# Kernel tuning notes

Measured on AMD Instinct MI355X. Metric: run time of the kernel, lower is better.

Reference implementation:

```python
import jax, jax.numpy as jnp
import numpy as np

WIDTH = 2048
NUM_HEADS = 16
HEAD_DIM = WIDTH // NUM_HEADS  # 128
ROPE_DIMS = HEAD_DIM // 2      # 64, partial rotary
WINDOW = 512
ROPE_BASE = 10000.0
NEG_INF = -1e9


def apply_rope(x, dims, offset=0, base=ROPE_BASE):
    # x: [B, H, L, hd]; non-traditional (half-split) rotary on first `dims` dims.
    L = x.shape[2]
    half = dims // 2
    pos = (offset + jnp.arange(L)).astype(x.dtype)                     # [L]
    inv_freq = jnp.exp(-jnp.log(jnp.asarray(base, x.dtype)) * (jnp.arange(0, dims, 2).astype(x.dtype) / dims))  # [half]
    theta = pos[:, None] * inv_freq[None, :]                           # [L, half]
    cos = jnp.cos(theta)[None, None]                                   # [1,1,L,half]
    sin = jnp.sin(theta)[None, None]
    x1 = x[..., :half]
    x2 = x[..., half:dims]
    rest = x[..., dims:]
    rx1 = x1 * cos - x2 * sin
    rx2 = x1 * sin + x2 * cos
    return jnp.concatenate([rx1, rx2, rest], axis=-1)


def setup_inputs() -> dict:
    key = jax.random.key(0)
    ks = jax.random.split(key, 6)
    B, L, D, hd = 2, 2048, WIDTH, HEAD_DIM
    x = jax.random.normal(ks[0], (B, L, D), dtype=jnp.float32)
    Wq = jax.random.normal(ks[1], (D, D), dtype=jnp.float32) * 0.02
    Wk = jax.random.normal(ks[2], (D, hd), dtype=jnp.float32) * 0.02
    Wv = jax.random.normal(ks[3], (D, hd), dtype=jnp.float32) * 0.02
    Wo = jax.random.normal(ks[4], (D, D), dtype=jnp.float32) * 0.02
    bo = jax.random.normal(ks[5], (D,), dtype=jnp.float32) * 0.02
    return {"x": x, "Wq": Wq, "Wk": Wk, "Wv": Wv, "Wo": Wo, "bo": bo}


def reference(x, Wq, Wk, Wv, Wo, bo):
    B, L, D = x.shape
    H, hd = NUM_HEADS, HEAD_DIM
    scale = hd ** (-0.5)

    q = (x @ Wq).reshape(B, L, H, hd).transpose(0, 2, 1, 3)   # [B,H,L,hd]
    k = (x @ Wk).reshape(B, L, 1, hd).transpose(0, 2, 1, 3)   # [B,1,L,hd] (MQA)
    v = (x @ Wv).reshape(B, L, 1, hd).transpose(0, 2, 1, 3)

    q = apply_rope(q, ROPE_DIMS)
    k = apply_rope(k, ROPE_DIMS)

    # sliding-window causal mask: attend iff 0 <= i - j < WINDOW
    i = jnp.arange(L)[:, None]
    j = jnp.arange(L)[None, :]
    allowed = (i - j >= 0) & (i - j < WINDOW)                  # [L,L]
    mask = jnp.where(allowed, 0.0, NEG_INF).astype(x.dtype)

    scores = jnp.einsum("bhqd,bkd->bhqk", q, k[:, 0]) * scale  # [B,H,L,L]
    scores = scores + mask[None, None]
    attn = jax.nn.softmax(scores, axis=-1)
    out = jnp.einsum("bhqk,bkd->bhqd", attn, v[:, 0])          # [B,H,L,hd]
    out = out.transpose(0, 2, 1, 3).reshape(B, L, D)
    return out @ Wo + bo
```

## Files before the change

kernel.cpp:

```cpp
#include <hip/hip_runtime.h>
#include <hip/hip_bf16.h>
#include <stdint.h>


typedef float  f32x4  __attribute__((ext_vector_type(4)));
typedef __bf16 bf16x8 __attribute__((ext_vector_type(8)));

#define ASYNC_LD16(gp, lp)                                                     \
  __builtin_amdgcn_global_load_lds(                                            \
      (__attribute__((address_space(1))) void*)(gp),                           \
      (__attribute__((address_space(3))) void*)(lp), 16, 0, 0)

__global__ __launch_bounds__(256) void prep_all(
    const float* __restrict__ x, __hip_bfloat16* __restrict__ xb,
    const float* __restrict__ Wq, const float* __restrict__ Wk,
    const float* __restrict__ Wv, const float* __restrict__ Wo,
    __hip_bfloat16* __restrict__ wqkvT, __hip_bfloat16* __restrict__ woT) {
  __shared__ float t[32][33];
  int bid = blockIdx.x;
  if (bid < 8192) {
    const int i = bid * 256 + threadIdx.x;
    const float4 v = ((const float4*)x)[i];
    __align__(8) __hip_bfloat16 o[4] = {
        __float2bfloat16(v.x), __float2bfloat16(v.y),
        __float2bfloat16(v.z), __float2bfloat16(v.w)};
    *(uint2*)(xb + (size_t)i * 4) = *(uint2*)o;
    return;
  }
  bid -= 8192;
  const float* src;
  __hip_bfloat16* dst;
  int C, cb, rb;
  if (bid < 4096) {
    src = Wq; dst = wqkvT; C = 2048; cb = bid & 63; rb = bid >> 6;
  } else if (bid < 4352) {
    const int l = bid - 4096;
    src = Wk; dst = wqkvT + 2048ull * 2048; C = 128; cb = l & 3; rb = l >> 2;
  } else if (bid < 4608) {
    const int l = bid - 4352;
    src = Wv; dst = wqkvT + 2176ull * 2048; C = 128; cb = l & 3; rb = l >> 2;
  } else {
    const int l = bid - 4608;
    src = Wo; dst = woT; C = 2048; cb = l & 63; rb = l >> 6;
  }
  const int c0 = cb * 32, r0 = rb * 32;
  const int xx = threadIdx.x & 31, y = threadIdx.x >> 5;
#pragma unroll
  for (int i = 0; i < 32; i += 8)
    t[y + i][xx] = src[(size_t)(r0 + y + i) * C + c0 + xx];
  __syncthreads();
#pragma unroll
  for (int i = 0; i < 32; i += 8)
    dst[(size_t)(c0 + y + i) * 2048 + r0 + xx] = __float2bfloat16(t[xx][y + i]);
}

__device__ __forceinline__ void xcd_remap(int& bx, int& by) {
  const int nwg = gridDim.x * gridDim.y;
  const int flat = blockIdx.y * gridDim.x + blockIdx.x;
  const int cpx = nwg >> 3;
  const int nid = (flat & 7) * cpx + (flat >> 3);
  bx = nid % gridDim.x;
  by = nid / gridDim.x;
}

__device__ __forceinline__ void gemm_core64(const __bf16* __restrict__ A,
                                            const __bf16* __restrict__ BT,
                                            int K, int m0, int n0, __bf16* As,
                                            __bf16* Bs, f32x4 (&acc)[2][4]) {
  const int tid = threadIdx.x;
  const int wave = tid >> 6;
  const int lane = tid & 63;
  const int wm = (wave & 3) * 32;
  const int wn = (wave >> 2) * 64;
  const int ln = lane & 15;
  const int quad = lane >> 4;
  const int rdoff = (quad ^ ((ln >> 1) & 3)) * 8;

  size_t goff[2];
  int ldsoff[2];
#pragma unroll
  for (int i = 0; i < 2; i++) {
    const int cidx = (wave * 2 + i) * 64 + lane;
    const int p = cidx >> 9;
    const int pidx = cidx & 511;
    const int row = pidx >> 2;
    const int cc = pidx & 3;
    const int cg = cc ^ ((row >> 1) & 3);
    goff[i] = (size_t)row * K + p * 32 + cg * 8;
    ldsoff[i] = (wave * 2 + i) * 512;
  }
  const __bf16* Abase = A + (size_t)m0 * K;
  const __bf16* Bbase = BT + (size_t)n0 * K;

  for (int k0 = 0; k0 < K; k0 += 64) {
#pragma unroll
    for (int i = 0; i < 2; i++)
      ASYNC_LD16(Abase + k0 + goff[i], As + ldsoff[i]);
#pragma unroll
    for (int i = 0; i < 2; i++)
      ASYNC_LD16(Bbase + k0 + goff[i], Bs + ldsoff[i]);
    __syncthreads();
    bf16x8 af[2][2], bf[4][2];
#pragma unroll
    for (int i = 0; i < 2; i++)
#pragma unroll
      for (int p = 0; p < 2; p++)
        af[i][p] = *(const bf16x8*)&As[p * 4096 + (wm + i * 16 + ln) * 32 + rdoff];
#pragma unroll
    for (int j = 0; j < 4; j++)
#pragma unroll
      for (int p = 0; p < 2; p++)
        bf[j][p] = *(const bf16x8*)&Bs[p * 4096 + (wn + j * 16 + ln) * 32 + rdoff];
#pragma unroll
    for (int p = 0; p < 2; p++)
#pragma unroll
      for (int i = 0; i < 2; i++)
#pragma unroll
        for (int j = 0; j < 4; j++)
          acc[i][j] = __builtin_amdgcn_mfma_f32_16x16x32_bf16(af[i][p], bf[j][p],
                                                              acc[i][j], 0, 0, 0);
    __syncthreads();
  }
}

__global__ __launch_bounds__(512) void gemm_qkv(
    const __bf16* __restrict__ A, const __bf16* __restrict__ BT,
    __hip_bfloat16* __restrict__ qd, __hip_bfloat16* __restrict__ kd,
    __hip_bfloat16* __restrict__ vtd, int K) {
  __shared__ __align__(16) __bf16 As[128 * 64];
  __shared__ __align__(16) __bf16 Bs[128 * 64];
  int bx, by;
  xcd_remap(bx, by);
  const int m0 = by * 128;
  const int n0 = bx * 128;
  f32x4 acc[2][4];
  const f32x4 zero = {0.f, 0.f, 0.f, 0.f};
#pragma unroll
  for (int i = 0; i < 2; i++)
#pragma unroll
    for (int j = 0; j < 4; j++) acc[i][j] = zero;
  gemm_core64(A, BT, K, m0, n0, As, Bs, acc);

  const int tid = threadIdx.x;
  const int wave = tid >> 6;
  const int lane = tid & 63;
  const int quad = lane >> 4;
  const int ln = lane & 15;
  const int wm = (wave & 3) * 32;
  const int wn = (wave >> 2) * 64;

  if (n0 == 2176) {
    const int bb = m0 >> 11;
    const int mloc = m0 & 2047;
#pragma unroll
    for (int i = 0; i < 2; i++) {
      const int rb = mloc + wm + i * 16 + quad * 4;
#pragma unroll
      for (int j = 0; j < 4; j++) {
        const int col = wn + j * 16 + ln;
        __align__(8) __hip_bfloat16 t4[4];
#pragma unroll
        for (int r = 0; r < 4; r++) t4[r] = __float2bfloat16(acc[i][j][r]);
        *(uint2*)(vtd + ((size_t)(bb * 128 + col)) * 2048 + rb) = *(uint2*)t4;
      }
    }
    return;
  }

  __hip_bfloat16* dst;
  int dstride, dcol;
  if (n0 < 2048) {
    dst = qd; dstride = 2048; dcol = n0;
  } else {
    dst = kd; dstride = 128; dcol = 0;
  }
  const bool dorope = (wn == 0);
  float invf0 = 0.f, invf1 = 0.f;
  if (dorope) {
    invf0 = expf(-0.28782313662425574f * (float)ln);
    invf1 = expf(-0.28782313662425574f * (float)(16 + ln));
  }

#pragma unroll
  for (int i = 0; i < 2; i++) {
#pragma unroll
    for (int r = 0; r < 4; r++) {
      const int row = m0 + wm + i * 16 + quad * 4 + r;
      float o0 = acc[i][0][r], o1 = acc[i][1][r];
      float o2 = acc[i][2][r], o3 = acc[i][3][r];
      if (dorope) {
        const float pos = (float)(row & 2047);
        float s0, c0, s1, c1;
        __sincosf(pos * invf0, &s0, &c0);
        __sincosf(pos * invf1, &s1, &c1);
        const float a0 = o0, b0 = o2, a1 = o1, b1 = o3;
        o0 = a0 * c0 - b0 * s0;
        o2 = a0 * s0 + b0 * c0;
        o1 = a1 * c1 - b1 * s1;
        o3 = a1 * s1 + b1 * c1;
      }
      __hip_bfloat16* rp = dst + (size_t)row * dstride + dcol + wn + ln;
      rp[0]  = __float2bfloat16(o0);
      rp[16] = __float2bfloat16(o1);
      rp[32] = __float2bfloat16(o2);
      rp[48] = __float2bfloat16(o3);
    }
  }
}

__global__ __launch_bounds__(512) void gemm_out(
    const __bf16* __restrict__ A, const __bf16* __restrict__ BT,
    float* __restrict__ C, const float* __restrict__ bias, int N, int K) {
  __shared__ __align__(16) __bf16 As[128 * 64];
  __shared__ __align__(16) __bf16 Bs[128 * 64];
  int bx, by;
  xcd_remap(bx, by);
  const int m0 = by * 128;
  const int n0 = bx * 128;
  f32x4 acc[2][4];
  const f32x4 zero = {0.f, 0.f, 0.f, 0.f};
#pragma unroll
  for (int i = 0; i < 2; i++)
#pragma unroll
    for (int j = 0; j < 4; j++) acc[i][j] = zero;
  gemm_core64(A, BT, K, m0, n0, As, Bs, acc);

  const int tid = threadIdx.x;
  const int wave = tid >> 6;
  const int lane = tid & 63;
  const int wm = (wave & 3) * 32;
  const int wn = (wave >> 2) * 64;
  const int lrow = lane & 15;
#pragma unroll
  for (int j = 0; j < 4; j++) {
    const int col = n0 + wn + j * 16 + lrow;
    const float bv = bias[col];
#pragma unroll
    for (int i = 0; i < 2; i++) {
#pragma unroll
      for (int r = 0; r < 4; r++) {
        const int row = m0 + wm + i * 16 + (lane >> 4) * 4 + r;
        C[(size_t)row * N + col] = acc[i][j][r] + bv;
      }
    }
  }
}

__global__ __launch_bounds__(256) void attn_mfma(
    const __bf16* __restrict__ qb,
    const __bf16* __restrict__ kb,
    const __bf16* __restrict__ vtb,
    __hip_bfloat16* __restrict__ o)
{
  __shared__ __align__(16) __bf16 Ks[4][64 * 32];
  __shared__ __align__(16) __bf16 Vs[2][128 * 32];
  __shared__ __align__(16) __bf16 Ps[4][2][2][512];
  const int tid = threadIdx.x;
  const int wave = tid >> 6;
  const int lane = tid & 63;
  const int quad = lane >> 4;
  const int ln = lane & 15;
  const int bid = blockIdx.x;
  const int q0 = (bid & 15) * 128;
  const int h = (bid >> 4) & 15;
  const int b = bid >> 8;
  const int swr = (ln >> 1) & 3;
  const int rdoff = (quad ^ swr) * 8;

  bf16x8 qf[2][4];
#pragma unroll
  for (int g = 0; g < 2; g++) {
    const __bf16* qrow =
        qb + ((size_t)(b * 2048 + q0 + wave * 32 + g * 16 + ln)) * 2048 + h * 128;
#pragma unroll
    for (int ks = 0; ks < 4; ks++)
      qf[g][ks] = *(const bf16x8*)(qrow + ks * 32 + quad * 8);
  }

  f32x4 oacc[2][8];
  const f32x4 zero = {0.f, 0.f, 0.f, 0.f};
#pragma unroll
  for (int g = 0; g < 2; g++)
#pragma unroll
    for (int nb = 0; nb < 8; nb++) oacc[g][nb] = zero;
  float li[2][4] = {{0.f, 0.f, 0.f, 0.f}, {0.f, 0.f, 0.f, 0.f}};
  const float scale = 0.08838834764831845f;

  const __bf16* kbase = kb + (size_t)b * 2048 * 128;
  const __bf16* vbase = vtb + (size_t)b * 128 * 2048;

  const int tstart = (q0 >= 512) ? 0 : (512 - q0) / 64;
  for (int t = tstart; t < 10; ++t) {
    const int jt = q0 - 512 + 64 * t;
    __syncthreads();
    {
      const int key4 = lane >> 2, uu = lane & 3;
      const int sw = (key4 >> 1) & 3;
#pragma unroll
      for (int i = 0; i < 4; ++i) {
        const int c = wave * 4 + i;
        const int ks = c & 3, keybase = (c >> 2) * 16;
        ASYNC_LD16(kbase + (size_t)(jt + keybase + key4) * 128 + ks * 32 +
                       (uu ^ sw) * 8,
                   &Ks[ks][keybase * 32]);
      }
#pragma unroll
      for (int i = 0; i < 4; ++i) {
        const int c = wave * 4 + i;
        const int p = c & 1, dbase = (c >> 1) * 16;
        ASYNC_LD16(vbase + (size_t)(dbase + key4) * 2048 + jt + p * 32 +
                       (uu ^ sw) * 8,
                   &Vs[p][dbase * 32]);
      }
    }
    __syncthreads();

    f32x4 sacc[2][4];
#pragma unroll
    for (int g = 0; g < 2; g++)
#pragma unroll
      for (int j = 0; j < 4; j++) sacc[g][j] = zero;
#pragma unroll
    for (int j = 0; j < 4; j++)
#pragma unroll
      for (int ks = 0; ks < 4; ks++) {
        const bf16x8 kf = *(const bf16x8*)&Ks[ks][(j * 16 + ln) * 32 + rdoff];
#pragma unroll
        for (int g = 0; g < 2; g++)
          sacc[g][j] = __builtin_amdgcn_mfma_f32_16x16x32_bf16(qf[g][ks], kf,
                                                               sacc[g][j], 0, 0, 0);
      }

#pragma unroll
    for (int g = 0; g < 2; g++)
#pragma unroll
      for (int j = 0; j < 4; j++)
#pragma unroll
        for (int r = 0; r < 4; r++) {
          float v = sacc[g][j][r] * scale;
          const int d0 = (wave * 32 + g * 16 + quad * 4 + r) - (j * 16 + ln);
          if (t <= 1 && d0 >= (t << 6)) v = -1e30f;
          if (t >= 8 && d0 < ((t - 8) << 6)) v = -1e30f;
          v = fminf(v, 60.f);
          const float p = __expf(v);
          li[g][r] += p;
          const int ch = (j & 1) * 2 + (ln >> 3);
          const int swp = (quad * 2 + (r >> 1)) & 3;
          Ps[wave][g][j >> 1]
            [(quad * 4 + r) * 32 + (ch ^ swp) * 8 + (ln & 7)] = (__bf16)p;
        }

    const bf16x8 pf00 = *(const bf16x8*)&Ps[wave][0][0][ln * 32 + rdoff];
    const bf16x8 pf01 = *(const bf16x8*)&Ps[wave][0][1][ln * 32 + rdoff];
    const bf16x8 pf10 = *(const bf16x8*)&Ps[wave][1][0][ln * 32 + rdoff];
    const bf16x8 pf11 = *(const bf16x8*)&Ps[wave][1][1][ln * 32 + rdoff];
#pragma unroll
    for (int nb = 0; nb < 8; nb++) {
      const bf16x8 vf0 = *(const bf16x8*)&Vs[0][(nb * 16 + ln) * 32 + rdoff];
      const bf16x8 vf1 = *(const bf16x8*)&Vs[1][(nb * 16 + ln) * 32 + rdoff];
      oacc[0][nb] =
          __builtin_amdgcn_mfma_f32_16x16x32_bf16(pf00, vf0, oacc[0][nb], 0, 0, 0);
      oacc[0][nb] =
          __builtin_amdgcn_mfma_f32_16x16x32_bf16(pf01, vf1, oacc[0][nb], 0, 0, 0);
      oacc[1][nb] =
          __builtin_amdgcn_mfma_f32_16x16x32_bf16(pf10, vf0, oacc[1][nb], 0, 0, 0);
      oacc[1][nb] =
          __builtin_amdgcn_mfma_f32_16x16x32_bf16(pf11, vf1, oacc[1][nb], 0, 0, 0);
    }
  }

#pragma unroll
  for (int off = 1; off < 16; off <<= 1)
#pragma unroll
    for (int g = 0; g < 2; g++)
#pragma unroll
      for (int r = 0; r < 4; r++) li[g][r] += __shfl_xor(li[g][r], off);

#pragma unroll
  for (int g = 0; g < 2; g++) {
    __hip_bfloat16* obase =
        o + ((size_t)(b * 2048 + q0 + wave * 32 + g * 16 + quad * 4)) * 2048 +
        h * 128 + ln;
#pragma unroll
    for (int r = 0; r < 4; r++) {
      const float inv = 1.0f / li[g][r];
#pragma unroll
      for (int nb = 0; nb < 8; nb++)
        obase[(size_t)r * 2048 + nb * 16] = __float2bfloat16(oacc[g][nb][r] * inv);
    }
  }
}

extern "C" void kernel_launch(void* const* d_in, const int* in_sizes, int n_in,
                              void* d_out, int out_size, void* d_ws,
                              size_t ws_size, hipStream_t stream) {
  const float* x = (const float*)d_in[0];
  const float* Wq = (const float*)d_in[1];
  const float* Wk = (const float*)d_in[2];
  const float* Wv = (const float*)d_in[3];
  const float* Wo = (const float*)d_in[4];
  const float* bo = (const float*)d_in[5];
  float* out = (float*)d_out;

  char* w = (char*)d_ws;
  auto alloc = [&](size_t bytes) {
    void* p = (void*)w;
    w += (bytes + 255) & ~(size_t)255;
    return p;
  };
  __bf16* xb = (__bf16*)alloc(4096ull * 2048 * 2);
  __hip_bfloat16* wqkvT = (__hip_bfloat16*)alloc(2304ull * 2048 * 2);
  __hip_bfloat16* woT = (__hip_bfloat16*)alloc(2048ull * 2048 * 2);
  __hip_bfloat16* qbuf = (__hip_bfloat16*)alloc(4096ull * 2048 * 2);
  __hip_bfloat16* kbuf = (__hip_bfloat16*)alloc(4096ull * 128 * 2);
  __hip_bfloat16* vtb = (__hip_bfloat16*)alloc(4096ull * 128 * 2);
  __hip_bfloat16* attnb = (__hip_bfloat16*)xb;

  prep_all<<<16896, 256, 0, stream>>>(x, (__hip_bfloat16*)xb, Wq, Wk, Wv, Wo,
                                      wqkvT, woT);

  gemm_qkv<<<dim3(18, 32), 512, 0, stream>>>(xb, (const __bf16*)wqkvT, qbuf,
                                             kbuf, vtb, 2048);

  attn_mfma<<<512, 256, 0, stream>>>((const __bf16*)qbuf, (const __bf16*)kbuf,
                                     (const __bf16*)vtb, attnb);

  gemm_out<<<dim3(16, 32), 512, 0, stream>>>((const __bf16*)attnb,
                                             (const __bf16*)woT, out, bo, 2048,
                                             2048);
}
```

Measured before the change: 264.3 us.

## Double-buffer LDS tiles in GEMMs and attention and specialize mask-free softmax

```diff
diff --git a/kernel.cpp b/kernel.cpp
--- a/kernel.cpp
+++ b/kernel.cpp
@@ -63,10 +63,10 @@
   by = nid / gridDim.x;
 }
 
-__device__ __forceinline__ void gemm_core64(const __bf16* __restrict__ A,
-                                            const __bf16* __restrict__ BT,
-                                            int K, int m0, int n0, __bf16* As,
-                                            __bf16* Bs, f32x4 (&acc)[2][4]) {
+__device__ __forceinline__ void gemm_core_db(const __bf16* __restrict__ A,
+                                             const __bf16* __restrict__ BT,
+                                             int K, int m0, int n0, __bf16* As,
+                                             __bf16* Bs, f32x4 (&acc)[2][4]) {
   const int tid = threadIdx.x;
   const int wave = tid >> 6;
   const int lane = tid & 63;
@@ -91,35 +91,51 @@
   }
   const __bf16* Abase = A + (size_t)m0 * K;
   const __bf16* Bbase = BT + (size_t)n0 * K;
-
-  for (int k0 = 0; k0 < K; k0 += 64) {
+  const int NT = K >> 6;
+
+#pragma unroll
+  for (int i = 0; i < 2; i++) ASYNC_LD16(Abase + goff[i], As + ldsoff[i]);
+#pragma unroll
+  for (int i = 0; i < 2; i++) ASYNC_LD16(Bbase + goff[i], Bs + ldsoff[i]);
+
+  int cur = 0;
+  for (int t = 0; t < NT; ++t) {
+    __syncthreads();
+    if (t + 1 < NT) {
+      const int k0 = (t + 1) << 6;
+      __bf16* an = As + ((cur ^ 1) << 13);
+      __bf16* bn = Bs + ((cur ^ 1) << 13);
+#pragma unroll
+      for (int i = 0; i < 2; i++)
+        ASYNC_LD16(Abase + k0 + goff[i], an + ldsoff[i]);
+#pragma unroll
+      for (int i = 0; i < 2; i++)
+        ASYNC_LD16(Bbase + k0 + goff[i], bn + ldsoff[i]);
+    }
+    const __bf16* as_ = As + (cur << 13);
+    const __bf16* bs_ = Bs + (cur << 13);
+    bf16x8 af[2][2], bfv[4][2];
 #pragma unroll
     for (int i = 0; i < 2; i++)
-      ASYNC_LD16(Abase + k0 + goff[i], As + ldsoff[i]);
-#pragma unroll
-    for (int i = 0; i < 2; i++)
-      ASYNC_LD16(Bbase + k0 + goff[i], Bs + ldsoff[i]);
-    __syncthreads();
-    bf16x8 af[2][2], bf[4][2];
-#pragma unroll
-    for (int i = 0; i < 2; i++)
 #pragma unroll
       for (int p = 0; p < 2; p++)
-        af[i][p] = *(const bf16x8*)&As[p * 4096 + (wm + i * 16 + ln) * 32 + rdoff];
+        af[i][p] =
+            *(const bf16x8*)&as_[p * 4096 + (wm + i * 16 + ln) * 32 + rdoff];
 #pragma unroll
     for (int j = 0; j < 4; j++)
 #pragma unroll
       for (int p = 0; p < 2; p++)
-        bf[j][p] = *(const bf16x8*)&Bs[p * 4096 + (wn + j * 16 + ln) * 32 + rdoff];
+        bfv[j][p] =
+            *(const bf16x8*)&bs_[p * 4096 + (wn + j * 16 + ln) * 32 + rdoff];
 #pragma unroll
     for (int p = 0; p < 2; p++)
 #pragma unroll
       for (int i = 0; i < 2; i++)
 #pragma unroll
         for (int j = 0; j < 4; j++)
-          acc[i][j] = __builtin_amdgcn_mfma_f32_16x16x32_bf16(af[i][p], bf[j][p],
-                                                              acc[i][j], 0, 0, 0);
-    __syncthreads();
+          acc[i][j] = __builtin_amdgcn_mfma_f32_16x16x32_bf16(
+              af[i][p], bfv[j][p], acc[i][j], 0, 0, 0);
+    cur ^= 1;
   }
 }
 
@@ -127,8 +143,8 @@
     const __bf16* __restrict__ A, const __bf16* __restrict__ BT,
     __hip_bfloat16* __restrict__ qd, __hip_bfloat16* __restrict__ kd,
     __hip_bfloat16* __restrict__ vtd, int K) {
-  __shared__ __align__(16) __bf16 As[128 * 64];
-  __shared__ __align__(16) __bf16 Bs[128 * 64];
+  __shared__ __align__(16) __bf16 As[2 * 8192];
+  __shared__ __align__(16) __bf16 Bs[2 * 8192];
   int bx, by;
   xcd_remap(bx, by);
   const int m0 = by * 128;
@@ -139,7 +155,7 @@
   for (int i = 0; i < 2; i++)
 #pragma unroll
     for (int j = 0; j < 4; j++) acc[i][j] = zero;
-  gemm_core64(A, BT, K, m0, n0, As, Bs, acc);
+  gemm_core_db(A, BT, K, m0, n0, As, Bs, acc);
 
   const int tid = threadIdx.x;
   const int wave = tid >> 6;
@@ -211,8 +227,8 @@
 __global__ __launch_bounds__(512) void gemm_out(
     const __bf16* __restrict__ A, const __bf16* __restrict__ BT,
     float* __restrict__ C, const float* __restrict__ bias, int N, int K) {
-  __shared__ __align__(16) __bf16 As[128 * 64];
-  __shared__ __align__(16) __bf16 Bs[128 * 64];
+  __shared__ __align__(16) __bf16 As[2 * 8192];
+  __shared__ __align__(16) __bf16 Bs[2 * 8192];
   int bx, by;
   xcd_remap(bx, by);
   const int m0 = by * 128;
@@ -223,7 +239,7 @@
   for (int i = 0; i < 2; i++)
 #pragma unroll
     for (int j = 0; j < 4; j++) acc[i][j] = zero;
-  gemm_core64(A, BT, K, m0, n0, As, Bs, acc);
+  gemm_core_db(A, BT, K, m0, n0, As, Bs, acc);
 
   const int tid = threadIdx.x;
   const int wave = tid >> 6;
@@ -252,8 +268,8 @@
     const __bf16* __restrict__ vtb,
     __hip_bfloat16* __restrict__ o)
 {
-  __shared__ __align__(16) __bf16 Ks[4][64 * 32];
-  __shared__ __align__(16) __bf16 Vs[2][128 * 32];
+  __shared__ __align__(16) __bf16 Ks[2][4][64 * 32];
+  __shared__ __align__(16) __bf16 Vs[2][2][128 * 32];
   __shared__ __align__(16) __bf16 Ps[4][2][2][512];
   const int tid = threadIdx.x;
   const int wave = tid >> 6;
@@ -289,85 +305,104 @@
   const __bf16* kbase = kb + (size_t)b * 2048 * 128;
   const __bf16* vbase = vtb + (size_t)b * 128 * 2048;
 
+  const int key4 = lane >> 2, uu = lane & 3;
+  const int sw = (key4 >> 1) & 3;
+
+  auto stage_kv = [&](int t, int bufi) {
+    const int jt = q0 - 512 + 64 * t;
+#pragma unroll
+    for (int i = 0; i < 4; ++i) {
+      const int c = wave * 4 + i;
+      const int ks = c & 3, keybase = (c >> 2) * 16;
+      ASYNC_LD16(kbase + (size_t)(jt + keybase + key4) * 128 + ks * 32 +
+                     (uu ^ sw) * 8,
+                 &Ks[bufi][ks][keybase * 32]);
+    }
+#pragma unroll
+    for (int i = 0; i < 4; ++i) {
+      const int c = wave * 4 + i;
+      const int p = c & 1, dbase = (c >> 1) * 16;
+      ASYNC_LD16(vbase + (size_t)(dbase + key4) * 2048 + jt + p * 32 +
+                     (uu ^ sw) * 8,
+                 &Vs[bufi][p][dbase * 32]);
+    }
+  };
+
+#define SOFTMAX_BODY(MASKED)                                                   \
+  _Pragma("unroll") for (int g = 0; g < 2; g++)                                \
+  _Pragma("unroll") for (int j = 0; j < 4; j++)                                \
+  _Pragma("unroll") for (int r = 0; r < 4; r++) {                              \
+    float v = sacc[g][j][r] * scale;                                           \
+    if (MASKED) {                                                              \
+      const int d0 = (wave * 32 + g * 16 + quad * 4 + r) - (j * 16 + ln);      \
+      if (t <= 1 && d0 >= (t << 6)) v = -1e30f;                                \
+      if (t >= 8 && d0 < ((t - 8) << 6)) v = -1e30f;                           \
+    }                                                                          \
+    v = fminf(v, 60.f);                                                        \
+    const float p = __expf(v);                                                 \
+    li[g][r] += p;                                                             \
+    const int ch = (j & 1) * 2 + (ln >> 3);                                    \
+    const int swp = (quad * 2 + (r >> 1)) & 3;                                 \
+    Ps[wave][g][j >> 1][(quad * 4 + r) * 32 + (ch ^ swp) * 8 + (ln & 7)] =     \
+        (__bf16)p;                                                             \
+  }
+
   const int tstart = (q0 >= 512) ? 0 : (512 - q0) / 64;
+  int cur = 0;
+  stage_kv(tstart, 0);
   for (int t = tstart; t < 10; ++t) {
-    const int jt = q0 - 512 + 64 * t;
     __syncthreads();
-    {
-      const int key4 = lane >> 2, uu = lane & 3;
-      const int sw = (key4 >> 1) & 3;
-#pragma unroll
-      for (int i = 0; i < 4; ++i) {
-        const int c = wave * 4 + i;
-        const int ks = c & 3, keybase = (c >> 2) * 16;
-        ASYNC_LD16(kbase + (size_t)(jt + keybase + key4) * 128 + ks * 32 +
-                       (uu ^ sw) * 8,
-                   &Ks[ks][keybase * 32]);
+    if (t + 1 < 10) stage_kv(t + 1, cur ^ 1);
+
+    f32x4 sacc[2][4];
+#pragma unroll
+    for (int g = 0; g < 2; g++)
+#pragma unroll
+      for (int j = 0; j < 4; j++) sacc[g][j] = zero;
+    __builtin_amdgcn_s_setprio(1);
+#pragma unroll
+    for (int j = 0; j < 4; j++)
+#pragma unroll
+      for (int ks = 0; ks < 4; ks++) {
+        const bf16x8 kf =
+            *(const bf16x8*)&Ks[cur][ks][(j * 16 + ln) * 32 + rdoff];
+#pragma unroll
+        for (int g = 0; g < 2; g++)
+          sacc[g][j] = __builtin_amdgcn_mfma_f32_16x16x32_bf16(
+              qf[g][ks], kf, sacc[g][j], 0, 0, 0);
       }
-#pragma unroll
-      for (int i = 0; i < 4; ++i) {
-        const int c = wave * 4 + i;
-        const int p = c & 1, dbase = (c >> 1) * 16;
-        ASYNC_LD16(vbase + (size_t)(dbase + key4) * 2048 + jt + p * 32 +
-                       (uu ^ sw) * 8,
-                   &Vs[p][dbase * 32]);
-      }
-    }
-    __syncthreads();
-
-    f32x4 sacc[2][4];
-#pragma unroll
-    for (int g = 0; g < 2; g++)
-#pragma unroll
-      for (int j = 0; j < 4; j++) sacc[g][j] = zero;
-#pragma unroll
-    for (int j = 0; j < 4; j++)
-#pragma unroll
-      for (int ks = 0; ks < 4; ks++) {
-        const bf16x8 kf = *(const bf16x8*)&Ks[ks][(j * 16 + ln) * 32 + rdoff];
-#pragma unroll
-        for (int g = 0; g < 2; g++)
-          sacc[g][j] = __builtin_amdgcn_mfma_f32_16x16x32_bf16(qf[g][ks], kf,
-                                                               sacc[g][j], 0, 0, 0);
-      }
-
-#pragma unroll
-    for (int g = 0; g < 2; g++)
-#pragma unroll
-      for (int j = 0; j < 4; j++)
-#pragma unroll
-        for (int r = 0; r < 4; r++) {
-          float v = sacc[g][j][r] * scale;
-          const int d0 = (wave * 32 + g * 16 + quad * 4 + r) - (j * 16 + ln);
-          if (t <= 1 && d0 >= (t << 6)) v = -1e30f;
-          if (t >= 8 && d0 < ((t - 8) << 6)) v = -1e30f;
-          v = fminf(v, 60.f);
-          const float p = __expf(v);
-          li[g][r] += p;
-          const int ch = (j & 1) * 2 + (ln >> 3);
-          const int swp = (quad * 2 + (r >> 1)) & 3;
-          Ps[wave][g][j >> 1]
-            [(quad * 4 + r) * 32 + (ch ^ swp) * 8 + (ln & 7)] = (__bf16)p;
-        }
+    __builtin_amdgcn_s_setprio(0);
+
+    if (t <= 1 || t >= 8) {
+      SOFTMAX_BODY(1)
+    } else {
+      SOFTMAX_BODY(0)
+    }
 
     const bf16x8 pf00 = *(const bf16x8*)&Ps[wave][0][0][ln * 32 + rdoff];
     const bf16x8 pf01 = *(const bf16x8*)&Ps[wave][0][1][ln * 32 + rdoff];
     const bf16x8 pf10 = *(const bf16x8*)&Ps[wave][1][0][ln * 32 + rdoff];
     const bf16x8 pf11 = *(const bf16x8*)&Ps[wave][1][1][ln * 32 + rdoff];
+    __builtin_amdgcn_s_setprio(1);
 #pragma unroll
     for (int nb = 0; nb < 8; nb++) {
-      const bf16x8 vf0 = *(const bf16x8*)&Vs[0][(nb * 16 + ln) * 32 + rdoff];
-      const bf16x8 vf1 = *(const bf16x8*)&Vs[1][(nb * 16 + ln) * 32 + rdoff];
-      oacc[0][nb] =
-          __builtin_amdgcn_mfma_f32_16x16x32_bf16(pf00, vf0, oacc[0][nb], 0, 0, 0);
-      oacc[0][nb] =
-          __builtin_amdgcn_mfma_f32_16x16x32_bf16(pf01, vf1, oacc[0][nb], 0, 0, 0);
-      oacc[1][nb] =
-          __builtin_amdgcn_mfma_f32_16x16x32_bf16(pf10, vf0, oacc[1][nb], 0, 0, 0);
-      oacc[1][nb] =
-          __builtin_amdgcn_mfma_f32_16x16x32_bf16(pf11, vf1, oacc[1][nb], 0, 0, 0);
-    }
-  }
+      const bf16x8 vf0 =
+          *(const bf16x8*)&Vs[cur][0][(nb * 16 + ln) * 32 + rdoff];
+      const bf16x8 vf1 =
+          *(const bf16x8*)&Vs[cur][1][(nb * 16 + ln) * 32 + rdoff];
+      oacc[0][nb] = __builtin_amdgcn_mfma_f32_16x16x32_bf16(pf00, vf0,
+                                                            oacc[0][nb], 0, 0, 0);
+      oacc[0][nb] = __builtin_amdgcn_mfma_f32_16x16x32_bf16(pf01, vf1,
+                                                            oacc[0][nb], 0, 0, 0);
+      oacc[1][nb] = __builtin_amdgcn_mfma_f32_16x16x32_bf16(pf10, vf0,
+                                                            oacc[1][nb], 0, 0, 0);
+      oacc[1][nb] = __builtin_amdgcn_mfma_f32_16x16x32_bf16(pf11, vf1,
+                                                            oacc[1][nb], 0, 0, 0);
+    }
+    __builtin_amdgcn_s_setprio(0);
+    cur ^= 1;
+  }
+#undef SOFTMAX_BODY
 
 #pragma unroll
   for (int off = 1; off < 16; off <<= 1)
```

Result: faster. 253.8 us (-4.0%).
